# Optimization experiments

Hardware: AMD Instinct MI355X
Metric: run time of the kernel (lower is better)

## Reference

```python
import jax, jax.numpy as jnp
import numpy as np

# Per-layer (in_dim, hidden) for the 6 stacked LSTM layers:
# rnn_inp: (1,64),(64,64),(64,64); rnn_out: (64,1),(1,1),(1,1)
_LAYER_DIMS = [(1, 64), (64, 64), (64, 64), (64, 1), (1, 1), (1, 1)]
_LAYER_NAMES = ['a0', 'a1', 'a2', 'b0', 'b1', 'b2']


def _lstm_layer(x, w_ih, w_hh, b_ih, b_hh):
    """Single unidirectional LSTM layer, PyTorch gate order (i, f, g, o).
    x: [B, T, Din]; w_ih: [4H, Din]; w_hh: [4H, H]; biases: [4H]. Returns [B, T, H]."""
    H = w_hh.shape[1]
    B = x.shape[0]
    # Input projection for all timesteps at once (one big GEMM).
    pre = jnp.einsum('btd,gd->btg', x, w_ih) + b_ih + b_hh  # [B, T, 4H]
    pre_t = jnp.swapaxes(pre, 0, 1)  # [T, B, 4H]

    def step(carry, xt):
        h, c = carry
        gates = xt + h @ w_hh.T  # [B, 4H]
        i, f, g, o = jnp.split(gates, 4, axis=-1)
        i = jax.nn.sigmoid(i)
        f = jax.nn.sigmoid(f)
        g = jnp.tanh(g)
        o = jax.nn.sigmoid(o)
        c = f * c + i * g
        h = o * jnp.tanh(c)
        return (h, c), h

    h0 = jnp.zeros((B, H), x.dtype)
    (_, _), hs = jax.lax.scan(step, (h0, h0), pre_t)  # hs: [T, B, H]
    return jnp.swapaxes(hs, 0, 1)


def setup_inputs() -> dict:
    key = jax.random.key(0)
    B, T = 256, 512
    inp = {}
    k, key = jax.random.split(key)
    inp['x'] = jax.random.normal(k, (B, T, 1), dtype=jnp.float32)
    for name, (din, h) in zip(_LAYER_NAMES, _LAYER_DIMS):
        s = 1.0 / np.sqrt(h)  # PyTorch LSTM init scale U(-1/sqrt(H), 1/sqrt(H))
        k1, k2, k3, k4, key = jax.random.split(key, 5)
        inp[f'w_ih_{name}'] = jax.random.uniform(k1, (4 * h, din), jnp.float32, -s, s)
        inp[f'w_hh_{name}'] = jax.random.uniform(k2, (4 * h, h), jnp.float32, -s, s)
        inp[f'b_ih_{name}'] = jax.random.uniform(k3, (4 * h,), jnp.float32, -s, s)
        inp[f'b_hh_{name}'] = jax.random.uniform(k4, (4 * h,), jnp.float32, -s, s)
    return inp


def reference(x,
              w_ih_a0, w_hh_a0, b_ih_a0, b_hh_a0,
              w_ih_a1, w_hh_a1, b_ih_a1, b_hh_a1,
              w_ih_a2, w_hh_a2, b_ih_a2, b_hh_a2,
              w_ih_b0, w_hh_b0, b_ih_b0, b_hh_b0,
              w_ih_b1, w_hh_b1, b_ih_b1, b_hh_b1,
              w_ih_b2, w_hh_b2, b_ih_b2, b_hh_b2):
    layers = [
        (w_ih_a0, w_hh_a0, b_ih_a0, b_hh_a0),
        (w_ih_a1, w_hh_a1, b_ih_a1, b_hh_a1),
        (w_ih_a2, w_hh_a2, b_ih_a2, b_hh_a2),
        (w_ih_b0, w_hh_b0, b_ih_b0, b_hh_b0),
        (w_ih_b1, w_hh_b1, b_ih_b1, b_hh_b1),
        (w_ih_b2, w_hh_b2, b_ih_b2, b_hh_b2),
    ]
    h = x
    for w_ih, w_hh, b_ih, b_hh in layers:
        h = _lstm_layer(h, w_ih, w_hh, b_ih, b_hh)
    # activation between the two LSTM stacks is identity (activation_type='identity')
    return h  # [B, T, 1]
```

## Files before the change

### kernel.cpp

```cpp
#include <hip/hip_runtime.h>


#define BB 256
#define TT 512
#define CH 8
#define NS 16

typedef _Float16 v2h __attribute__((ext_vector_type(2)));

__device__ __forceinline__ float sig_(float x) {
  return __builtin_amdgcn_rcpf(1.f + __builtin_amdgcn_exp2f(-1.44269504f * x));
}
__device__ __forceinline__ float tanh_(float x) {
  return __builtin_fmaf(2.f, __builtin_amdgcn_rcpf(1.f + __builtin_amdgcn_exp2f(-2.88539008f * x)), -1.f);
}

template <int K>
__device__ __forceinline__ float qb_(float v) {
  return __int_as_float(__builtin_amdgcn_update_dpp(
      0, __float_as_int(v), (K | (K << 2) | (K << 4) | (K << 6)), 0xF, 0xF, true));
}

__device__ __forceinline__ void ldsbar_() {
  asm volatile("s_waitcnt lgkmcnt(0)\n\ts_barrier" ::: "memory");
}

#if __has_builtin(__builtin_amdgcn_fdot2)
#define FDOT2(acc, a, b) (acc) = __builtin_amdgcn_fdot2((a), (b), (acc), false)
#else
#define FDOT2(acc, a, b) \
  (acc) = __builtin_fmaf((float)(a)[0], (float)(b)[0], \
          __builtin_fmaf((float)(a)[1], (float)(b)[1], (acc)))
#endif
#define KEEPP(a) asm volatile("" : "+v"(a))
#define PIN16(w)                                                            \
  do {                                                                      \
    _Pragma("unroll") for (int _i = 0; _i < 16; ++_i) KEEPP((w)[_i]);       \
  } while (0)

__device__ __forceinline__ v2h bc2h_(int v) { return __builtin_bit_cast(v2h, v); }
__device__ __forceinline__ int pk2_(float x, float y) {
  return __builtin_bit_cast(int, v2h{(_Float16)x, (_Float16)y});
}

__device__ __forceinline__ void load_h64(const _Float16* p, v2h hv[32]) {
  const int4* hp = reinterpret_cast<const int4*>(p);
#pragma unroll
  for (int i = 0; i < 8; ++i) {
    int4 blk = hp[i];
    hv[4 * i + 0] = bc2h_(blk.x);
    hv[4 * i + 1] = bc2h_(blk.y);
    hv[4 * i + 2] = bc2h_(blk.z);
    hv[4 * i + 3] = bc2h_(blk.w);
  }
}

__device__ __forceinline__ void load_row_pair(const float* src, v2h lo[16], v2h hi[16]) {
  const float4* p = reinterpret_cast<const float4*>(src);
#pragma unroll
  for (int i = 0; i < 8; ++i) {
    float4 v = p[i];
    lo[2 * i]     = v2h{(_Float16)v.x, (_Float16)v.y};
    lo[2 * i + 1] = v2h{(_Float16)v.z, (_Float16)v.w};
  }
#pragma unroll
  for (int i = 0; i < 8; ++i) {
    float4 v = p[8 + i];
    hi[2 * i]     = v2h{(_Float16)v.x, (_Float16)v.y};
    hi[2 * i + 1] = v2h{(_Float16)v.z, (_Float16)v.w};
  }
}

__device__ __forceinline__ void load_rec_w(const float* W, int lane,
                                           v2h wt[4][16], unsigned char* wl) {
#pragma unroll
  for (int q = 0; q < 4; ++q) {
    const int row = q * 64 + lane;
    const float4* p = reinterpret_cast<const float4*>(W + row * 64);
#pragma unroll
    for (int i = 0; i < 8; ++i) {
      float4 v = p[i];
      wt[q][2 * i]     = v2h{(_Float16)v.x, (_Float16)v.y};
      wt[q][2 * i + 1] = v2h{(_Float16)v.z, (_Float16)v.w};
    }
#pragma unroll
    for (int i = 0; i < 4; ++i) {
      float4 va = p[8 + 2 * i], vb = p[9 + 2 * i];
      int4 blk;
      blk.x = pk2_(va.x, va.y); blk.y = pk2_(va.z, va.w);
      blk.z = pk2_(vb.x, vb.y); blk.w = pk2_(vb.z, vb.w);
      *reinterpret_cast<int4*>(wl + row * 80 + i * 16) = blk;
    }
  }
}

__device__ __forceinline__ void dot4full_(const v2h wt[4][16],
                                          const unsigned char* wl, int lane,
                                          const v2h hv[32],
                                          float& p0, float& p1, float& p2, float& p3) {
  float a0 = p0, a1 = p1, a2 = p2, a3 = p3;
  float b0 = 0.f, b1 = 0.f, b2 = 0.f, b3 = 0.f;
#pragma unroll
  for (int j = 0; j < 16; j += 2) {
    FDOT2(a0, wt[0][j], hv[j]);         FDOT2(a1, wt[1][j], hv[j]);
    FDOT2(a2, wt[2][j], hv[j]);         FDOT2(a3, wt[3][j], hv[j]);
    FDOT2(b0, wt[0][j + 1], hv[j + 1]); FDOT2(b1, wt[1][j + 1], hv[j + 1]);
    FDOT2(b2, wt[2][j + 1], hv[j + 1]); FDOT2(b3, wt[3][j + 1], hv[j + 1]);
  }
  const int rb0 = lane * 80, rb1 = (64 + lane) * 80,
            rb2 = (128 + lane) * 80, rb3 = (192 + lane) * 80;
#pragma unroll
  for (int jb = 0; jb < 4; ++jb) {
    int4 w0 = *reinterpret_cast<const int4*>(wl + rb0 + jb * 16);
    int4 w1 = *reinterpret_cast<const int4*>(wl + rb1 + jb * 16);
    int4 w2 = *reinterpret_cast<const int4*>(wl + rb2 + jb * 16);
    int4 w3 = *reinterpret_cast<const int4*>(wl + rb3 + jb * 16);
    const int h0 = 16 + jb * 4;
    FDOT2(a0, bc2h_(w0.x), hv[h0 + 0]); FDOT2(b0, bc2h_(w0.y), hv[h0 + 1]);
    FDOT2(a0, bc2h_(w0.z), hv[h0 + 2]); FDOT2(b0, bc2h_(w0.w), hv[h0 + 3]);
    FDOT2(a1, bc2h_(w1.x), hv[h0 + 0]); FDOT2(b1, bc2h_(w1.y), hv[h0 + 1]);
    FDOT2(a1, bc2h_(w1.z), hv[h0 + 2]); FDOT2(b1, bc2h_(w1.w), hv[h0 + 3]);
    FDOT2(a2, bc2h_(w2.x), hv[h0 + 0]); FDOT2(b2, bc2h_(w2.y), hv[h0 + 1]);
    FDOT2(a2, bc2h_(w2.z), hv[h0 + 2]); FDOT2(b2, bc2h_(w2.w), hv[h0 + 3]);
    FDOT2(a3, bc2h_(w3.x), hv[h0 + 0]); FDOT2(b3, bc2h_(w3.y), hv[h0 + 1]);
    FDOT2(a3, bc2h_(w3.z), hv[h0 + 2]); FDOT2(b3, bc2h_(w3.w), hv[h0 + 3]);
  }
  p0 = a0 + b0; p1 = a1 + b1; p2 = a2 + b2; p3 = a3 + b3;
}

__device__ __forceinline__ void dot2g_(const v2h* wa_lo, const v2h* wa_hi,
                                       const v2h* wb_lo, const v2h* wb_hi,
                                       const v2h hv[32], float& p0, float& p1) {
  float a0 = 0.f, a1 = 0.f, b0 = 0.f, b1 = 0.f;
#pragma unroll
  for (int j = 0; j < 16; j += 2) {
    FDOT2(a0, wa_lo[j], hv[j]);          FDOT2(b0, wa_lo[j + 1], hv[j + 1]);
    FDOT2(a0, wa_hi[j], hv[16 + j]);     FDOT2(b0, wa_hi[j + 1], hv[17 + j]);
    FDOT2(a1, wb_lo[j], hv[j]);          FDOT2(b1, wb_lo[j + 1], hv[j + 1]);
    FDOT2(a1, wb_hi[j], hv[16 + j]);     FDOT2(b1, wb_hi[j + 1], hv[17 + j]);
  }
  p0 = a0 + b0; p1 = a1 + b1;
}

__global__ __attribute__((amdgpu_flat_work_group_size(512, 512),
                          amdgpu_waves_per_eu(2, 2)))
void lstm_pipe_k(
    const float* __restrict__ x,
    const float* __restrict__ wih_a0, const float* __restrict__ whh_a0,
    const float* __restrict__ bih_a0, const float* __restrict__ bhh_a0,
    const float* __restrict__ wih_a1, const float* __restrict__ whh_a1,
    const float* __restrict__ bih_a1, const float* __restrict__ bhh_a1,
    const float* __restrict__ wih_a2, const float* __restrict__ whh_a2,
    const float* __restrict__ bih_a2, const float* __restrict__ bhh_a2,
    const float* __restrict__ wih_b0, const float* __restrict__ whh_b0,
    const float* __restrict__ bih_b0, const float* __restrict__ bhh_b0,
    const float* __restrict__ wih_b1, const float* __restrict__ whh_b1,
    const float* __restrict__ bih_b1, const float* __restrict__ bhh_b1,
    const float* __restrict__ wih_b2, const float* __restrict__ whh_b2,
    const float* __restrict__ bih_b2, const float* __restrict__ bhh_b2,
    float* __restrict__ out)
{
  const int b = blockIdx.x;
  const int tid = threadIdx.x;
  const int wave = tid >> 6;
  const int lane = tid & 63;

  __shared__ __align__(16) _Float16 hh[3][NS][64];
  __shared__ __align__(16) float pj[2][NS][256];
  __shared__ __align__(16) unsigned char wlds[3][256 * 80];
  __shared__ float xs[TT];

  for (int i = tid; i < TT; i += 512) xs[i] = x[(size_t)b * TT + i];
  for (int i = tid; i < 3 * NS * 64 / 2; i += 512) reinterpret_cast<int*>(hh)[i] = 0;

  v2h wt[4][16];
  float bias[4] = {0.f, 0.f, 0.f, 0.f};
  float wi0_[4] = {0.f, 0.f, 0.f, 0.f};
  float whb0[4] = {}, wi1b[4] = {}, wh1b[4] = {}, bb1[4] = {},
        wi2b[4] = {}, wh2b[4] = {}, bb2[4] = {};

  if (wave == 0) {
    load_rec_w(whh_a0, lane, wt, &wlds[0][0]);
#pragma unroll
    for (int q = 0; q < 4; ++q) {
      const int row = q * 64 + lane;
      bias[q] = bih_a0[row] + bhh_a0[row];
      wi0_[q] = wih_a0[row];
    }
    PIN16(wt[0]); PIN16(wt[1]); PIN16(wt[2]); PIN16(wt[3]);
  } else if (wave == 1) {
    load_rec_w(whh_a1, lane, wt, &wlds[1][0]);
#pragma unroll
    for (int q = 0; q < 4; ++q) {
      const int row = q * 64 + lane;
      bias[q] = bih_a1[row] + bhh_a1[row];
    }
    PIN16(wt[0]); PIN16(wt[1]); PIN16(wt[2]); PIN16(wt[3]);
  } else if (wave == 2) {
    load_rec_w(whh_a2, lane, wt, &wlds[2][0]);
#pragma unroll
    for (int q = 0; q < 4; ++q) {
      const int row = q * 64 + lane;
      bias[q] = bih_a2[row] + bhh_a2[row];
    }
    PIN16(wt[0]); PIN16(wt[1]); PIN16(wt[2]); PIN16(wt[3]);
  } else if (wave == 3) {
    const int q = lane & 3;
    load_row_pair(wih_b0 + q * 64, wt[0], wt[1]);
    bias[0] = bih_b0[q] + bhh_b0[q];
#pragma unroll
    for (int k = 0; k < 4; ++k) {
      whb0[k] = whh_b0[k];
      wi1b[k] = wih_b1[k]; wh1b[k] = whh_b1[k]; bb1[k] = bih_b1[k] + bhh_b1[k];
      wi2b[k] = wih_b2[k]; wh2b[k] = whh_b2[k]; bb2[k] = bih_b2[k] + bhh_b2[k];
    }
    PIN16(wt[0]); PIN16(wt[1]);
  } else if (wave == 4) {
    load_row_pair(wih_a1 + (0 * 64 + lane) * 64, wt[0], wt[1]);
    load_row_pair(wih_a1 + (1 * 64 + lane) * 64, wt[2], wt[3]);
    PIN16(wt[0]); PIN16(wt[1]); PIN16(wt[2]); PIN16(wt[3]);
  } else if (wave == 5) {
    load_row_pair(wih_a1 + (2 * 64 + lane) * 64, wt[0], wt[1]);
    load_row_pair(wih_a1 + (3 * 64 + lane) * 64, wt[2], wt[3]);
    PIN16(wt[0]); PIN16(wt[1]); PIN16(wt[2]); PIN16(wt[3]);
  } else if (wave == 6) {
    load_row_pair(wih_a2 + (0 * 64 + lane) * 64, wt[0], wt[1]);
    load_row_pair(wih_a2 + (1 * 64 + lane) * 64, wt[2], wt[3]);
    PIN16(wt[0]); PIN16(wt[1]); PIN16(wt[2]); PIN16(wt[3]);
  } else {
    load_row_pair(wih_a2 + (2 * 64 + lane) * 64, wt[0], wt[1]);
    load_row_pair(wih_a2 + (3 * 64 + lane) * 64, wt[2], wt[3]);
    PIN16(wt[0]); PIN16(wt[1]); PIN16(wt[2]); PIN16(wt[3]);
  }
  __syncthreads();

  float c = 0.f;
  float h0b = 0.f, c0b = 0.f, h1b = 0.f, c1b = 0.f, h2b = 0.f, c2b = 0.f;

  const int NE = TT / CH + 5;
  for (int e = 0; e < NE; ++e) {
    if (wave == 0) {
      const int t0 = e * CH;
      if (t0 < TT) {
        __builtin_amdgcn_s_setprio(1);
        for (int s = 0; s < CH; ++s) {
          const int t = t0 + s;
          v2h hv[32];
          load_h64(&hh[0][(t + NS - 1) & (NS - 1)][0], hv);
          const float xv = xs[t];
          float p0 = bias[0], p1 = bias[1], p2 = bias[2], p3 = bias[3];
          dot4full_(wt, &wlds[0][0], lane, hv, p0, p1, p2, p3);
          p0 = __builtin_fmaf(wi0_[0], xv, p0);
          p1 = __builtin_fmaf(wi0_[1], xv, p1);
          p2 = __builtin_fmaf(wi0_[2], xv, p2);
          p3 = __builtin_fmaf(wi0_[3], xv, p3);
          float gi = sig_(p0), gf = sig_(p1), gg = tanh_(p2), go = sig_(p3);
          c = __builtin_fmaf(gf, c, gi * gg);
          hh[0][t & (NS - 1)][lane] = (_Float16)(go * tanh_(c));
        }
        __builtin_amdgcn_s_setprio(0);
      }
    } else if (wave == 1) {
      const int t0 = (e - 2) * CH;
      if (t0 >= 0 && t0 < TT) {
        __builtin_amdgcn_s_setprio(1);
        for (int s = 0; s < CH; ++s) {
          const int t = t0 + s;
          v2h hv[32];
          load_h64(&hh[1][(t + NS - 1) & (NS - 1)][0], hv);
          float4 pr = *reinterpret_cast<const float4*>(&pj[0][t & (NS - 1)][lane * 4]);
          float p0 = bias[0], p1 = bias[1], p2 = bias[2], p3 = bias[3];
          dot4full_(wt, &wlds[1][0], lane, hv, p0, p1, p2, p3);
          p0 += pr.x; p1 += pr.y; p2 += pr.z; p3 += pr.w;
          float gi = sig_(p0), gf = sig_(p1), gg = tanh_(p2), go = sig_(p3);
          c = __builtin_fmaf(gf, c, gi * gg);
          hh[1][t & (NS - 1)][lane] = (_Float16)(go * tanh_(c));
        }
        __builtin_amdgcn_s_setprio(0);
      }
    } else if (wave == 2) {
      const int t0 = (e - 4) * CH;
      if (t0 >= 0 && t0 < TT) {
        __builtin_amdgcn_s_setprio(1);
        for (int s = 0; s < CH; ++s) {
          const int t = t0 + s;
          v2h hv[32];
          load_h64(&hh[2][(t + NS - 1) & (NS - 1)][0], hv);
          float4 pr = *reinterpret_cast<const float4*>(&pj[1][t & (NS - 1)][lane * 4]);
          float p0 = bias[0], p1 = bias[1], p2 = bias[2], p3 = bias[3];
          dot4full_(wt, &wlds[2][0], lane, hv, p0, p1, p2, p3);
          p0 += pr.x; p1 += pr.y; p2 += pr.z; p3 += pr.w;
          float gi = sig_(p0), gf = sig_(p1), gg = tanh_(p2), go = sig_(p3);
          c = __builtin_fmaf(gf, c, gi * gg);
          hh[2][t & (NS - 1)][lane] = (_Float16)(go * tanh_(c));
        }
        __builtin_amdgcn_s_setprio(0);
      }
    } else if (wave == 3) {
      const int t0 = (e - 5) * CH;
      if (t0 >= 0 && t0 < TT) {
        for (int s = 0; s < CH; ++s) {
          const int t = t0 + s;
          v2h hv[32];
          load_h64(&hh[2][t & (NS - 1)][0], hv);
          float pga = bias[0], pgb = 0.f;
#pragma unroll
          for (int j = 0; j < 16; ++j) {
            FDOT2(pga, wt[0][j], hv[j]);
            FDOT2(pgb, wt[1][j], hv[16 + j]);
          }
          float pg = pga + pgb;
          float p_i = qb_<0>(pg), p_f = qb_<1>(pg), p_g = qb_<2>(pg), p_o = qb_<3>(pg);
          float i0 = sig_(__builtin_fmaf(whb0[0], h0b, p_i));
          float f0 = sig_(__builtin_fmaf(whb0[1], h0b, p_f));
          float g0 = tanh_(__builtin_fmaf(whb0[2], h0b, p_g));
          float o0 = sig_(__builtin_fmaf(whb0[3], h0b, p_o));
          c0b = __builtin_fmaf(f0, c0b, i0 * g0);
          h0b = o0 * tanh_(c0b);
          float i1 = sig_(bb1[0] + __builtin_fmaf(wi1b[0], h0b, wh1b[0] * h1b));
          float f1 = sig_(bb1[1] + __builtin_fmaf(wi1b[1], h0b, wh1b[1] * h1b));
          float g1 = tanh_(bb1[2] + __builtin_fmaf(wi1b[2], h0b, wh1b[2] * h1b));
          float o1 = sig_(bb1[3] + __builtin_fmaf(wi1b[3], h0b, wh1b[3] * h1b));
          c1b = __builtin_fmaf(f1, c1b, i1 * g1);
          h1b = o1 * tanh_(c1b);
          float i2 = sig_(bb2[0] + __builtin_fmaf(wi2b[0], h1b, wh2b[0] * h2b));
          float f2 = sig_(bb2[1] + __builtin_fmaf(wi2b[1], h1b, wh2b[1] * h2b));
          float g2 = tanh_(bb2[2] + __builtin_fmaf(wi2b[2], h1b, wh2b[2] * h2b));
          float o2 = sig_(bb2[3] + __builtin_fmaf(wi2b[3], h1b, wh2b[3] * h2b));
          c2b = __builtin_fmaf(f2, c2b, i2 * g2);
          h2b = o2 * tanh_(c2b);
          if (lane == 0) out[(size_t)b * TT + t] = h2b;
        }
      }
    } else if (wave == 4) {
      const int t0 = (e - 1) * CH;
      if (t0 >= 0 && t0 < TT) {
        for (int s = 0; s < CH; ++s) {
          const int t = t0 + s;
          v2h hv[32];
          load_h64(&hh[0][t & (NS - 1)][0], hv);
          float p0, p1;
          dot2g_(wt[0], wt[1], wt[2], wt[3], hv, p0, p1);
          *reinterpret_cast<float2*>(&pj[0][t & (NS - 1)][lane * 4]) = float2{p0, p1};
        }
      }
    } else if (wave == 5) {
      const int t0 = (e - 1) * CH;
      if (t0 >= 0 && t0 < TT) {
        for (int s = 0; s < CH; ++s) {
          const int t = t0 + s;
          v2h hv[32];
          load_h64(&hh[0][t & (NS - 1)][0], hv);
          float p2, p3;
          dot2g_(wt[0], wt[1], wt[2], wt[3], hv, p2, p3);
          *reinterpret_cast<float2*>(&pj[0][t & (NS - 1)][lane * 4 + 2]) = float2{p2, p3};
        }
      }
    } else if (wave == 6) {
      const int t0 = (e - 3) * CH;
      if (t0 >= 0 && t0 < TT) {
        for (int s = 0; s < CH; ++s) {
          const int t = t0 + s;
          v2h hv[32];
          load_h64(&hh[1][t & (NS - 1)][0], hv);
          float p0, p1;
          dot2g_(wt[0], wt[1], wt[2], wt[3], hv, p0, p1);
          *reinterpret_cast<float2*>(&pj[1][t & (NS - 1)][lane * 4]) = float2{p0, p1};
        }
      }
    } else {
      const int t0 = (e - 3) * CH;
      if (t0 >= 0 && t0 < TT) {
        for (int s = 0; s < CH; ++s) {
          const int t = t0 + s;
          v2h hv[32];
          load_h64(&hh[1][t & (NS - 1)][0], hv);
          float p2, p3;
          dot2g_(wt[0], wt[1], wt[2], wt[3], hv, p2, p3);
          *reinterpret_cast<float2*>(&pj[1][t & (NS - 1)][lane * 4 + 2]) = float2{p2, p3};
        }
      }
    }
    ldsbar_();
  }
}

extern "C" void kernel_launch(void* const* d_in, const int* in_sizes, int n_in,
                              void* d_out, int out_size, void* d_ws, size_t ws_size,
                              hipStream_t stream) {
  const float* x      = (const float*)d_in[0];
  const float* wih_a0 = (const float*)d_in[1];
  const float* whh_a0 = (const float*)d_in[2];
  const float* bih_a0 = (const float*)d_in[3];
  const float* bhh_a0 = (const float*)d_in[4];
  const float* wih_a1 = (const float*)d_in[5];
  const float* whh_a1 = (const float*)d_in[6];
  const float* bih_a1 = (const float*)d_in[7];
  const float* bhh_a1 = (const float*)d_in[8];
  const float* wih_a2 = (const float*)d_in[9];
  const float* whh_a2 = (const float*)d_in[10];
  const float* bih_a2 = (const float*)d_in[11];
  const float* bhh_a2 = (const float*)d_in[12];
  const float* wih_b0 = (const float*)d_in[13];
  const float* whh_b0 = (const float*)d_in[14];
  const float* bih_b0 = (const float*)d_in[15];
  const float* bhh_b0 = (const float*)d_in[16];
  const float* wih_b1 = (const float*)d_in[17];
  const float* whh_b1 = (const float*)d_in[18];
  const float* bih_b1 = (const float*)d_in[19];
  const float* bhh_b1 = (const float*)d_in[20];
  const float* wih_b2 = (const float*)d_in[21];
  const float* whh_b2 = (const float*)d_in[22];
  const float* bih_b2 = (const float*)d_in[23];
  const float* bhh_b2 = (const float*)d_in[24];
  float* out = (float*)d_out;

  lstm_pipe_k<<<BB, 512, 0, stream>>>(
      x,
      wih_a0, whh_a0, bih_a0, bhh_a0,
      wih_a1, whh_a1, bih_a1, bhh_a1,
      wih_a2, whh_a2, bih_a2, bhh_a2,
      wih_b0, whh_b0, bih_b0, bhh_b0,
      wih_b1, whh_b1, bih_b1, bhh_b1,
      wih_b2, whh_b2, bih_b2, bhh_b2,
      out);
}
```

Baseline: 410.4 us.

## Compute recurrent LSTM matvec with MFMA 16x16x32 f16 instead of fdot2

The three 64-hidden recurrent waves now hold the whole W_hh in registers as MFMA B fragments (16 tiles x 2 k-chunks). Each step does 32 MFMA instructions against the broadcast previous h, then selects each lane's four gate values from the accumulators. The shared-memory weight spill and the fdot2 chains go away. In exchange, 15 of 16 rows of each MFMA are wasted work, MFMA latency sits on the serial recurrence path, and register pressure grows.

```diff
diff --git a/kernel.cpp b/kernel.cpp
--- a/kernel.cpp
+++ b/kernel.cpp
@@ -7,6 +7,8 @@
 #define NS 16
 
 typedef _Float16 v2h __attribute__((ext_vector_type(2)));
+typedef _Float16 v8h __attribute__((ext_vector_type(8)));
+typedef float v4f __attribute__((ext_vector_type(4)));
 
 __device__ __forceinline__ float sig_(float x) {
   return __builtin_amdgcn_rcpf(1.f + __builtin_amdgcn_exp2f(-1.44269504f * x));
@@ -39,9 +41,6 @@
   } while (0)
 
 __device__ __forceinline__ v2h bc2h_(int v) { return __builtin_bit_cast(v2h, v); }
-__device__ __forceinline__ int pk2_(float x, float y) {
-  return __builtin_bit_cast(int, v2h{(_Float16)x, (_Float16)y});
-}
 
 __device__ __forceinline__ void load_h64(const _Float16* p, v2h hv[32]) {
   const int4* hp = reinterpret_cast<const int4*>(p);
@@ -71,61 +70,41 @@
   }
 }
 
-__device__ __forceinline__ void load_rec_w(const float* W, int lane,
-                                           v2h wt[4][16], unsigned char* wl) {
-#pragma unroll
-  for (int q = 0; q < 4; ++q) {
-    const int row = q * 64 + lane;
-    const float4* p = reinterpret_cast<const float4*>(W + row * 64);
-#pragma unroll
-    for (int i = 0; i < 8; ++i) {
-      float4 v = p[i];
-      wt[q][2 * i]     = v2h{(_Float16)v.x, (_Float16)v.y};
-      wt[q][2 * i + 1] = v2h{(_Float16)v.z, (_Float16)v.w};
-    }
-#pragma unroll
-    for (int i = 0; i < 4; ++i) {
-      float4 va = p[8 + 2 * i], vb = p[9 + 2 * i];
-      int4 blk;
-      blk.x = pk2_(va.x, va.y); blk.y = pk2_(va.z, va.w);
-      blk.z = pk2_(vb.x, vb.y); blk.w = pk2_(vb.z, vb.w);
-      *reinterpret_cast<int4*>(wl + row * 80 + i * 16) = blk;
-    }
-  }
-}
-
-__device__ __forceinline__ void dot4full_(const v2h wt[4][16],
-                                          const unsigned char* wl, int lane,
-                                          const v2h hv[32],
-                                          float& p0, float& p1, float& p2, float& p3) {
-  float a0 = p0, a1 = p1, a2 = p2, a3 = p3;
-  float b0 = 0.f, b1 = 0.f, b2 = 0.f, b3 = 0.f;
-#pragma unroll
-  for (int j = 0; j < 16; j += 2) {
-    FDOT2(a0, wt[0][j], hv[j]);         FDOT2(a1, wt[1][j], hv[j]);
-    FDOT2(a2, wt[2][j], hv[j]);         FDOT2(a3, wt[3][j], hv[j]);
-    FDOT2(b0, wt[0][j + 1], hv[j + 1]); FDOT2(b1, wt[1][j + 1], hv[j + 1]);
-    FDOT2(b2, wt[2][j + 1], hv[j + 1]); FDOT2(b3, wt[3][j + 1], hv[j + 1]);
-  }
-  const int rb0 = lane * 80, rb1 = (64 + lane) * 80,
-            rb2 = (128 + lane) * 80, rb3 = (192 + lane) * 80;
-#pragma unroll
-  for (int jb = 0; jb < 4; ++jb) {
-    int4 w0 = *reinterpret_cast<const int4*>(wl + rb0 + jb * 16);
-    int4 w1 = *reinterpret_cast<const int4*>(wl + rb1 + jb * 16);
-    int4 w2 = *reinterpret_cast<const int4*>(wl + rb2 + jb * 16);
-    int4 w3 = *reinterpret_cast<const int4*>(wl + rb3 + jb * 16);
-    const int h0 = 16 + jb * 4;
-    FDOT2(a0, bc2h_(w0.x), hv[h0 + 0]); FDOT2(b0, bc2h_(w0.y), hv[h0 + 1]);
-    FDOT2(a0, bc2h_(w0.z), hv[h0 + 2]); FDOT2(b0, bc2h_(w0.w), hv[h0 + 3]);
-    FDOT2(a1, bc2h_(w1.x), hv[h0 + 0]); FDOT2(b1, bc2h_(w1.y), hv[h0 + 1]);
-    FDOT2(a1, bc2h_(w1.z), hv[h0 + 2]); FDOT2(b1, bc2h_(w1.w), hv[h0 + 3]);
-    FDOT2(a2, bc2h_(w2.x), hv[h0 + 0]); FDOT2(b2, bc2h_(w2.y), hv[h0 + 1]);
-    FDOT2(a2, bc2h_(w2.z), hv[h0 + 2]); FDOT2(b2, bc2h_(w2.w), hv[h0 + 3]);
-    FDOT2(a3, bc2h_(w3.x), hv[h0 + 0]); FDOT2(b3, bc2h_(w3.y), hv[h0 + 1]);
-    FDOT2(a3, bc2h_(w3.z), hv[h0 + 2]); FDOT2(b3, bc2h_(w3.w), hv[h0 + 3]);
-  }
-  p0 = a0 + b0; p1 = a1 + b1; p2 = a2 + b2; p3 = a3 + b3;
+__device__ __forceinline__ v8h ldbfrag_(const float* W, int t, int kc, int lane) {
+  const int row = 16 * t + (lane & 15);
+  const float* p = W + row * 64 + 32 * kc + 4 * (lane >> 4);
+  float4 fa = *reinterpret_cast<const float4*>(p);
+  float4 fb = *reinterpret_cast<const float4*>(p + 16);
+  return v8h{(_Float16)fa.x, (_Float16)fa.y, (_Float16)fa.z, (_Float16)fa.w,
+             (_Float16)fb.x, (_Float16)fb.y, (_Float16)fb.z, (_Float16)fb.w};
+}
+
+__device__ __forceinline__ void mfma_matvec_(const v8h bfr[16][2],
+                                             const _Float16* hprev, int lane,
+                                             float p[4]) {
+  const char* hp = reinterpret_cast<const char*>(hprev);
+  const int off = 8 * (lane >> 4);
+  int2 r00 = *reinterpret_cast<const int2*>(hp + off);
+  int2 r01 = *reinterpret_cast<const int2*>(hp + off + 32);
+  int2 r10 = *reinterpret_cast<const int2*>(hp + off + 64);
+  int2 r11 = *reinterpret_cast<const int2*>(hp + off + 96);
+  v8h A0 = __builtin_bit_cast(v8h, int4{r00.x, r00.y, r01.x, r01.y});
+  v8h A1 = __builtin_bit_cast(v8h, int4{r10.x, r10.y, r11.x, r11.y});
+  const v4f z = {0.f, 0.f, 0.f, 0.f};
+  v4f acc[16];
+#pragma unroll
+  for (int t = 0; t < 16; ++t) {
+    v4f d = __builtin_amdgcn_mfma_f32_16x16x32_f16(A0, bfr[t][0], z, 0, 0, 0);
+    acc[t] = __builtin_amdgcn_mfma_f32_16x16x32_f16(A1, bfr[t][1], d, 0, 0, 0);
+  }
+  const int q = lane >> 4;
+  const bool s0 = q & 1, s1 = q & 2;
+#pragma unroll
+  for (int g = 0; g < 4; ++g) {
+    float v01 = s0 ? acc[4 * g + 1][0] : acc[4 * g + 0][0];
+    float v23 = s0 ? acc[4 * g + 3][0] : acc[4 * g + 2][0];
+    p[g] = s1 ? v23 : v01;
+  }
 }
 
 __device__ __forceinline__ void dot2g_(const v2h* wa_lo, const v2h* wa_hi,
@@ -167,12 +146,12 @@
 
   __shared__ __align__(16) _Float16 hh[3][NS][64];
   __shared__ __align__(16) float pj[2][NS][256];
-  __shared__ __align__(16) unsigned char wlds[3][256 * 80];
   __shared__ float xs[TT];
 
   for (int i = tid; i < TT; i += 512) xs[i] = x[(size_t)b * TT + i];
   for (int i = tid; i < 3 * NS * 64 / 2; i += 512) reinterpret_cast<int*>(hh)[i] = 0;
 
+  v8h bfr[16][2];
   v2h wt[4][16];
   float bias[4] = {0.f, 0.f, 0.f, 0.f};
   float wi0_[4] = {0.f, 0.f, 0.f, 0.f};
@@ -180,30 +159,33 @@
         wi2b[4] = {}, wh2b[4] = {}, bb2[4] = {};
 
   if (wave == 0) {
-    load_rec_w(whh_a0, lane, wt, &wlds[0][0]);
+#pragma unroll
+    for (int t = 0; t < 16; ++t) {
+      bfr[t][0] = ldbfrag_(whh_a0, t, 0, lane);
+      bfr[t][1] = ldbfrag_(whh_a0, t, 1, lane);
+    }
 #pragma unroll
     for (int q = 0; q < 4; ++q) {
       const int row = q * 64 + lane;
       bias[q] = bih_a0[row] + bhh_a0[row];
       wi0_[q] = wih_a0[row];
     }
-    PIN16(wt[0]); PIN16(wt[1]); PIN16(wt[2]); PIN16(wt[3]);
   } else if (wave == 1) {
-    load_rec_w(whh_a1, lane, wt, &wlds[1][0]);
-#pragma unroll
-    for (int q = 0; q < 4; ++q) {
-      const int row = q * 64 + lane;
-      bias[q] = bih_a1[row] + bhh_a1[row];
-    }
-    PIN16(wt[0]); PIN16(wt[1]); PIN16(wt[2]); PIN16(wt[3]);
+#pragma unroll
+    for (int t = 0; t < 16; ++t) {
+      bfr[t][0] = ldbfrag_(whh_a1, t, 0, lane);
+      bfr[t][1] = ldbfrag_(whh_a1, t, 1, lane);
+    }
+#pragma unroll
+    for (int q = 0; q < 4; ++q) bias[q] = bih_a1[q * 64 + lane] + bhh_a1[q * 64 + lane];
   } else if (wave == 2) {
-    load_rec_w(whh_a2, lane, wt, &wlds[2][0]);
-#pragma unroll
-    for (int q = 0; q < 4; ++q) {
-      const int row = q * 64 + lane;
-      bias[q] = bih_a2[row] + bhh_a2[row];
-    }
-    PIN16(wt[0]); PIN16(wt[1]); PIN16(wt[2]); PIN16(wt[3]);
+#pragma unroll
+    for (int t = 0; t < 16; ++t) {
+      bfr[t][0] = ldbfrag_(whh_a2, t, 0, lane);
+      bfr[t][1] = ldbfrag_(whh_a2, t, 1, lane);
+    }
+#pragma unroll
+    for (int q = 0; q < 4; ++q) bias[q] = bih_a2[q * 64 + lane] + bhh_a2[q * 64 + lane];
   } else if (wave == 3) {
     const int q = lane & 3;
     load_row_pair(wih_b0 + q * 64, wt[0], wt[1]);
@@ -245,15 +227,13 @@
         __builtin_amdgcn_s_setprio(1);
         for (int s = 0; s < CH; ++s) {
           const int t = t0 + s;
-          v2h hv[32];
-          load_h64(&hh[0][(t + NS - 1) & (NS - 1)][0], hv);
           const float xv = xs[t];
-          float p0 = bias[0], p1 = bias[1], p2 = bias[2], p3 = bias[3];
-          dot4full_(wt, &wlds[0][0], lane, hv, p0, p1, p2, p3);
-          p0 = __builtin_fmaf(wi0_[0], xv, p0);
-          p1 = __builtin_fmaf(wi0_[1], xv, p1);
-          p2 = __builtin_fmaf(wi0_[2], xv, p2);
-          p3 = __builtin_fmaf(wi0_[3], xv, p3);
+          float p[4];
+          mfma_matvec_(bfr, &hh[0][(t + NS - 1) & (NS - 1)][0], lane, p);
+          float p0 = __builtin_fmaf(wi0_[0], xv, p[0] + bias[0]);
+          float p1 = __builtin_fmaf(wi0_[1], xv, p[1] + bias[1]);
+          float p2 = __builtin_fmaf(wi0_[2], xv, p[2] + bias[2]);
+          float p3 = __builtin_fmaf(wi0_[3], xv, p[3] + bias[3]);
           float gi = sig_(p0), gf = sig_(p1), gg = tanh_(p2), go = sig_(p3);
           c = __builtin_fmaf(gf, c, gi * gg);
           hh[0][t & (NS - 1)][lane] = (_Float16)(go * tanh_(c));
@@ -266,12 +246,13 @@
         __builtin_amdgcn_s_setprio(1);
         for (int s = 0; s < CH; ++s) {
           const int t = t0 + s;
-          v2h hv[32];
-          load_h64(&hh[1][(t + NS - 1) & (NS - 1)][0], hv);
           float4 pr = *reinterpret_cast<const float4*>(&pj[0][t & (NS - 1)][lane * 4]);
-          float p0 = bias[0], p1 = bias[1], p2 = bias[2], p3 = bias[3];
-          dot4full_(wt, &wlds[1][0], lane, hv, p0, p1, p2, p3);
-          p0 += pr.x; p1 += pr.y; p2 += pr.z; p3 += pr.w;
+          float p[4];
+          mfma_matvec_(bfr, &hh[1][(t + NS - 1) & (NS - 1)][0], lane, p);
+          float p0 = p[0] + bias[0] + pr.x;
+          float p1 = p[1] + bias[1] + pr.y;
+          float p2 = p[2] + bias[2] + pr.z;
+          float p3 = p[3] + bias[3] + pr.w;
           float gi = sig_(p0), gf = sig_(p1), gg = tanh_(p2), go = sig_(p3);
           c = __builtin_fmaf(gf, c, gi * gg);
           hh[1][t & (NS - 1)][lane] = (_Float16)(go * tanh_(c));
@@ -284,12 +265,13 @@
         __builtin_amdgcn_s_setprio(1);
         for (int s = 0; s < CH; ++s) {
           const int t = t0 + s;
-          v2h hv[32];
-          load_h64(&hh[2][(t + NS - 1) & (NS - 1)][0], hv);
           float4 pr = *reinterpret_cast<const float4*>(&pj[1][t & (NS - 1)][lane * 4]);
-          float p0 = bias[0], p1 = bias[1], p2 = bias[2], p3 = bias[3];
-          dot4full_(wt, &wlds[2][0], lane, hv, p0, p1, p2, p3);
-          p0 += pr.x; p1 += pr.y; p2 += pr.z; p3 += pr.w;
+          float p[4];
+          mfma_matvec_(bfr, &hh[2][(t + NS - 1) & (NS - 1)][0], lane, p);
+          float p0 = p[0] + bias[0] + pr.x;
+          float p1 = p[1] + bias[1] + pr.y;
+          float p2 = p[2] + bias[2] + pr.z;
+          float p3 = p[3] + bias[3] + pr.w;
           float gi = sig_(p0), gf = sig_(p1), gg = tanh_(p2), go = sig_(p3);
           c = __builtin_fmaf(gf, c, gi * gg);
           hh[2][t & (NS - 1)][lane] = (_Float16)(go * tanh_(c));
```

After: 583.8 us. +42.2%, slower.

## Replace block-wide barrier pipeline with per-wave LDS progress flags

Applied to the files above, without the earlier changes.

The lockstep epoch loop, which ended every chunk with s_barrier across all eight waves, is replaced by per-wave progress counters in shared memory. Each wave spins on acquire loads until its producers have finished the chunk it needs and its consumers have freed ring slots, then posts its own progress with a release store. This lets each pipeline stage run ahead independently instead of waiting for the slowest wave every chunk, which should shorten the critical path through the wave-0 recurrence. The cost is busy-wait polling that takes issue slots on the SIMDs, plus the risk of ordering bugs in the ring-buffer dependencies.

```diff
diff --git a/kernel.cpp b/kernel.cpp
--- a/kernel.cpp
+++ b/kernel.cpp
@@ -5,6 +5,7 @@
 #define TT 512
 #define CH 8
 #define NS 16
+#define NW (TT / CH)
 
 typedef _Float16 v2h __attribute__((ext_vector_type(2)));
 
@@ -19,10 +20,6 @@
 __device__ __forceinline__ float qb_(float v) {
   return __int_as_float(__builtin_amdgcn_update_dpp(
       0, __float_as_int(v), (K | (K << 2) | (K << 4) | (K << 6)), 0xF, 0xF, true));
-}
-
-__device__ __forceinline__ void ldsbar_() {
-  asm volatile("s_waitcnt lgkmcnt(0)\n\ts_barrier" ::: "memory");
 }
 
 #if __has_builtin(__builtin_amdgcn_fdot2)
@@ -36,6 +33,17 @@
 #define PIN16(w)                                                            \
   do {                                                                      \
     _Pragma("unroll") for (int _i = 0; _i < 16; ++_i) KEEPP((w)[_i]);       \
+  } while (0)
+
+#define WAITP(i, v)                                                           \
+  while (__hip_atomic_load(&prog[i], __ATOMIC_ACQUIRE,                        \
+                           __HIP_MEMORY_SCOPE_WORKGROUP) < (v)) {}
+#define POSTP(i, v)                                                           \
+  do {                                                                        \
+    asm volatile("s_waitcnt lgkmcnt(0)" ::: "memory");                        \
+    if (lane == 0)                                                            \
+      __hip_atomic_store(&prog[i], (v), __ATOMIC_RELEASE,                     \
+                         __HIP_MEMORY_SCOPE_WORKGROUP);                       \
   } while (0)
 
 __device__ __forceinline__ v2h bc2h_(int v) { return __builtin_bit_cast(v2h, v); }
@@ -169,9 +177,11 @@
   __shared__ __align__(16) float pj[2][NS][256];
   __shared__ __align__(16) unsigned char wlds[3][256 * 80];
   __shared__ float xs[TT];
+  __shared__ int prog[8];
 
   for (int i = tid; i < TT; i += 512) xs[i] = x[(size_t)b * TT + i];
   for (int i = tid; i < 3 * NS * 64 / 2; i += 512) reinterpret_cast<int*>(hh)[i] = 0;
+  if (tid < 8) prog[tid] = 0;
 
   v2h wt[4][16];
   float bias[4] = {0.f, 0.f, 0.f, 0.f};
@@ -191,18 +201,12 @@
   } else if (wave == 1) {
     load_rec_w(whh_a1, lane, wt, &wlds[1][0]);
 #pragma unroll
-    for (int q = 0; q < 4; ++q) {
-      const int row = q * 64 + lane;
-      bias[q] = bih_a1[row] + bhh_a1[row];
-    }
+    for (int q = 0; q < 4; ++q) bias[q] = bih_a1[q * 64 + lane] + bhh_a1[q * 64 + lane];
     PIN16(wt[0]); PIN16(wt[1]); PIN16(wt[2]); PIN16(wt[3]);
   } else if (wave == 2) {
     load_rec_w(whh_a2, lane, wt, &wlds[2][0]);
 #pragma unroll
-    for (int q = 0; q < 4; ++q) {
-      const int row = q * 64 + lane;
-      bias[q] = bih_a2[row] + bhh_a2[row];
-    }
+    for (int q = 0; q < 4; ++q) bias[q] = bih_a2[q * 64 + lane] + bhh_a2[q * 64 + lane];
     PIN16(wt[0]); PIN16(wt[1]); PIN16(wt[2]); PIN16(wt[3]);
   } else if (wave == 3) {
     const int q = lane & 3;
@@ -237,151 +241,169 @@
   float c = 0.f;
   float h0b = 0.f, c0b = 0.f, h1b = 0.f, c1b = 0.f, h2b = 0.f, c2b = 0.f;
 
-  const int NE = TT / CH + 5;
-  for (int e = 0; e < NE; ++e) {
-    if (wave == 0) {
-      const int t0 = e * CH;
-      if (t0 < TT) {
-        __builtin_amdgcn_s_setprio(1);
-        for (int s = 0; s < CH; ++s) {
-          const int t = t0 + s;
-          v2h hv[32];
-          load_h64(&hh[0][(t + NS - 1) & (NS - 1)][0], hv);
-          const float xv = xs[t];
-          float p0 = bias[0], p1 = bias[1], p2 = bias[2], p3 = bias[3];
-          dot4full_(wt, &wlds[0][0], lane, hv, p0, p1, p2, p3);
-          p0 = __builtin_fmaf(wi0_[0], xv, p0);
-          p1 = __builtin_fmaf(wi0_[1], xv, p1);
-          p2 = __builtin_fmaf(wi0_[2], xv, p2);
-          p3 = __builtin_fmaf(wi0_[3], xv, p3);
-          float gi = sig_(p0), gf = sig_(p1), gg = tanh_(p2), go = sig_(p3);
-          c = __builtin_fmaf(gf, c, gi * gg);
-          hh[0][t & (NS - 1)][lane] = (_Float16)(go * tanh_(c));
+  if (wave == 0) {
+    __builtin_amdgcn_s_setprio(1);
+    for (int k = 0; k < NW; ++k) {
+      if (k >= 2) { WAITP(4, k - 1); WAITP(5, k - 1); }
+      const int t0 = k * CH;
+      for (int s = 0; s < CH; ++s) {
+        const int t = t0 + s;
+        v2h hv[32];
+        load_h64(&hh[0][(t + NS - 1) & (NS - 1)][0], hv);
+        const float xv = xs[t];
+        float p0 = bias[0], p1 = bias[1], p2 = bias[2], p3 = bias[3];
+        dot4full_(wt, &wlds[0][0], lane, hv, p0, p1, p2, p3);
+        p0 = __builtin_fmaf(wi0_[0], xv, p0);
+        p1 = __builtin_fmaf(wi0_[1], xv, p1);
+        p2 = __builtin_fmaf(wi0_[2], xv, p2);
+        p3 = __builtin_fmaf(wi0_[3], xv, p3);
+        float gi = sig_(p0), gf = sig_(p1), gg = tanh_(p2), go = sig_(p3);
+        c = __builtin_fmaf(gf, c, gi * gg);
+        hh[0][t & (NS - 1)][lane] = (_Float16)(go * tanh_(c));
+      }
+      POSTP(0, k + 1);
+    }
+    __builtin_amdgcn_s_setprio(0);
+  } else if (wave == 1) {
+    __builtin_amdgcn_s_setprio(1);
+    for (int k = 0; k < NW; ++k) {
+      WAITP(4, k + 1); WAITP(5, k + 1);
+      if (k >= 2) { WAITP(6, k - 1); WAITP(7, k - 1); }
+      const int t0 = k * CH;
+      for (int s = 0; s < CH; ++s) {
+        const int t = t0 + s;
+        v2h hv[32];
+        load_h64(&hh[1][(t + NS - 1) & (NS - 1)][0], hv);
+        float4 pr = *reinterpret_cast<const float4*>(&pj[0][t & (NS - 1)][lane * 4]);
+        float p0 = bias[0], p1 = bias[1], p2 = bias[2], p3 = bias[3];
+        dot4full_(wt, &wlds[1][0], lane, hv, p0, p1, p2, p3);
+        p0 += pr.x; p1 += pr.y; p2 += pr.z; p3 += pr.w;
+        float gi = sig_(p0), gf = sig_(p1), gg = tanh_(p2), go = sig_(p3);
+        c = __builtin_fmaf(gf, c, gi * gg);
+        hh[1][t & (NS - 1)][lane] = (_Float16)(go * tanh_(c));
+      }
+      POSTP(1, k + 1);
+    }
+    __builtin_amdgcn_s_setprio(0);
+  } else if (wave == 2) {
+    __builtin_amdgcn_s_setprio(1);
+    for (int k = 0; k < NW; ++k) {
+      WAITP(6, k + 1); WAITP(7, k + 1);
+      if (k >= 2) { WAITP(3, k - 1); }
+      const int t0 = k * CH;
+      for (int s = 0; s < CH; ++s) {
+        const int t = t0 + s;
+        v2h hv[32];
+        load_h64(&hh[2][(t + NS - 1) & (NS - 1)][0], hv);
+        float4 pr = *reinterpret_cast<const float4*>(&pj[1][t & (NS - 1)][lane * 4]);
+        float p0 = bias[0], p1 = bias[1], p2 = bias[2], p3 = bias[3];
+        dot4full_(wt, &wlds[2][0], lane, hv, p0, p1, p2, p3);
+        p0 += pr.x; p1 += pr.y; p2 += pr.z; p3 += pr.w;
+        float gi = sig_(p0), gf = sig_(p1), gg = tanh_(p2), go = sig_(p3);
+        c = __builtin_fmaf(gf, c, gi * gg);
+        hh[2][t & (NS - 1)][lane] = (_Float16)(go * tanh_(c));
+      }
+      POSTP(2, k + 1);
+    }
+    __builtin_amdgcn_s_setprio(0);
+  } else if (wave == 3) {
+    for (int k = 0; k < NW; ++k) {
+      WAITP(2, k + 1);
+      const int t0 = k * CH;
+      for (int s = 0; s < CH; ++s) {
+        const int t = t0 + s;
+        v2h hv[32];
+        load_h64(&hh[2][t & (NS - 1)][0], hv);
+        float pga = bias[0], pgb = 0.f;
+#pragma unroll
+        for (int j = 0; j < 16; ++j) {
+          FDOT2(pga, wt[0][j], hv[j]);
+          FDOT2(pgb, wt[1][j], hv[16 + j]);
         }
-        __builtin_amdgcn_s_setprio(0);
-      }
-    } else if (wave == 1) {
-      const int t0 = (e - 2) * CH;
-      if (t0 >= 0 && t0 < TT) {
-        __builtin_amdgcn_s_setprio(1);
-        for (int s = 0; s < CH; ++s) {
-          const int t = t0 + s;
-          v2h hv[32];
-          load_h64(&hh[1][(t + NS - 1) & (NS - 1)][0], hv);
-          float4 pr = *reinterpret_cast<const float4*>(&pj[0][t & (NS - 1)][lane * 4]);
-          float p0 = bias[0], p1 = bias[1], p2 = bias[2], p3 = bias[3];
-          dot4full_(wt, &wlds[1][0], lane, hv, p0, p1, p2, p3);
-          p0 += pr.x; p1 += pr.y; p2 += pr.z; p3 += pr.w;
-          float gi = sig_(p0), gf = sig_(p1), gg = tanh_(p2), go = sig_(p3);
-          c = __builtin_fmaf(gf, c, gi * gg);
-          hh[1][t & (NS - 1)][lane] = (_Float16)(go * tanh_(c));
-        }
-        __builtin_amdgcn_s_setprio(0);
-      }
-    } else if (wave == 2) {
-      const int t0 = (e - 4) * CH;
-      if (t0 >= 0 && t0 < TT) {
-        __builtin_amdgcn_s_setprio(1);
-        for (int s = 0; s < CH; ++s) {
-          const int t = t0 + s;
-          v2h hv[32];
-          load_h64(&hh[2][(t + NS - 1) & (NS - 1)][0], hv);
-          float4 pr = *reinterpret_cast<const float4*>(&pj[1][t & (NS - 1)][lane * 4]);
-          float p0 = bias[0], p1 = bias[1], p2 = bias[2], p3 = bias[3];
-          dot4full_(wt, &wlds[2][0], lane, hv, p0, p1, p2, p3);
-          p0 += pr.x; p1 += pr.y; p2 += pr.z; p3 += pr.w;
-          float gi = sig_(p0), gf = sig_(p1), gg = tanh_(p2), go = sig_(p3);
-          c = __builtin_fmaf(gf, c, gi * gg);
-          hh[2][t & (NS - 1)][lane] = (_Float16)(go * tanh_(c));
-        }
-        __builtin_amdgcn_s_setprio(0);
-      }
-    } else if (wave == 3) {
-      const int t0 = (e - 5) * CH;
-      if (t0 >= 0 && t0 < TT) {
-        for (int s = 0; s < CH; ++s) {
-          const int t = t0 + s;
-          v2h hv[32];
-          load_h64(&hh[2][t & (NS - 1)][0], hv);
-          float pga = bias[0], pgb = 0.f;
-#pragma unroll
-          for (int j = 0; j < 16; ++j) {
-            FDOT2(pga, wt[0][j], hv[j]);
-            FDOT2(pgb, wt[1][j], hv[16 + j]);
-          }
-          float pg = pga + pgb;
-          float p_i = qb_<0>(pg), p_f = qb_<1>(pg), p_g = qb_<2>(pg), p_o = qb_<3>(pg);
-          float i0 = sig_(__builtin_fmaf(whb0[0], h0b, p_i));
-          float f0 = sig_(__builtin_fmaf(whb0[1], h0b, p_f));
-          float g0 = tanh_(__builtin_fmaf(whb0[2], h0b, p_g));
-          float o0 = sig_(__builtin_fmaf(whb0[3], h0b, p_o));
-          c0b = __builtin_fmaf(f0, c0b, i0 * g0);
-          h0b = o0 * tanh_(c0b);
-          float i1 = sig_(bb1[0] + __builtin_fmaf(wi1b[0], h0b, wh1b[0] * h1b));
-          float f1 = sig_(bb1[1] + __builtin_fmaf(wi1b[1], h0b, wh1b[1] * h1b));
-          float g1 = tanh_(bb1[2] + __builtin_fmaf(wi1b[2], h0b, wh1b[2] * h1b));
-          float o1 = sig_(bb1[3] + __builtin_fmaf(wi1b[3], h0b, wh1b[3] * h1b));
-          c1b = __builtin_fmaf(f1, c1b, i1 * g1);
-          h1b = o1 * tanh_(c1b);
-          float i2 = sig_(bb2[0] + __builtin_fmaf(wi2b[0], h1b, wh2b[0] * h2b));
-          float f2 = sig_(bb2[1] + __builtin_fmaf(wi2b[1], h1b, wh2b[1] * h2b));
-          float g2 = tanh_(bb2[2] + __builtin_fmaf(wi2b[2], h1b, wh2b[2] * h2b));
-          float o2 = sig_(bb2[3] + __builtin_fmaf(wi2b[3], h1b, wh2b[3] * h2b));
-          c2b = __builtin_fmaf(f2, c2b, i2 * g2);
-          h2b = o2 * tanh_(c2b);
-          if (lane == 0) out[(size_t)b * TT + t] = h2b;
-        }
-      }
-    } else if (wave == 4) {
-      const int t0 = (e - 1) * CH;
-      if (t0 >= 0 && t0 < TT) {
-        for (int s = 0; s < CH; ++s) {
-          const int t = t0 + s;
-          v2h hv[32];
-          load_h64(&hh[0][t & (NS - 1)][0], hv);
-          float p0, p1;
-          dot2g_(wt[0], wt[1], wt[2], wt[3], hv, p0, p1);
-          *reinterpret_cast<float2*>(&pj[0][t & (NS - 1)][lane * 4]) = float2{p0, p1};
-        }
-      }
-    } else if (wave == 5) {
-      const int t0 = (e - 1) * CH;
-      if (t0 >= 0 && t0 < TT) {
-        for (int s = 0; s < CH; ++s) {
-          const int t = t0 + s;
-          v2h hv[32];
-          load_h64(&hh[0][t & (NS - 1)][0], hv);
-          float p2, p3;
-          dot2g_(wt[0], wt[1], wt[2], wt[3], hv, p2, p3);
-          *reinterpret_cast<float2*>(&pj[0][t & (NS - 1)][lane * 4 + 2]) = float2{p2, p3};
-        }
-      }
-    } else if (wave == 6) {
-      const int t0 = (e - 3) * CH;
-      if (t0 >= 0 && t0 < TT) {
-        for (int s = 0; s < CH; ++s) {
-          const int t = t0 + s;
-          v2h hv[32];
-          load_h64(&hh[1][t & (NS - 1)][0], hv);
-          float p0, p1;
-          dot2g_(wt[0], wt[1], wt[2], wt[3], hv, p0, p1);
-          *reinterpret_cast<float2*>(&pj[1][t & (NS - 1)][lane * 4]) = float2{p0, p1};
-        }
-      }
-    } else {
-      const int t0 = (e - 3) * CH;
-      if (t0 >= 0 && t0 < TT) {
-        for (int s = 0; s < CH; ++s) {
-          const int t = t0 + s;
-          v2h hv[32];
-          load_h64(&hh[1][t & (NS - 1)][0], hv);
-          float p2, p3;
-          dot2g_(wt[0], wt[1], wt[2], wt[3], hv, p2, p3);
-          *reinterpret_cast<float2*>(&pj[1][t & (NS - 1)][lane * 4 + 2]) = float2{p2, p3};
-        }
-      }
-    }
-    ldsbar_();
+        float pg = pga + pgb;
+        float p_i = qb_<0>(pg), p_f = qb_<1>(pg), p_g = qb_<2>(pg), p_o = qb_<3>(pg);
+        float i0 = sig_(__builtin_fmaf(whb0[0], h0b, p_i));
+        float f0 = sig_(__builtin_fmaf(whb0[1], h0b, p_f));
+        float g0 = tanh_(__builtin_fmaf(whb0[2], h0b, p_g));
+        float o0 = sig_(__builtin_fmaf(whb0[3], h0b, p_o));
+        c0b = __builtin_fmaf(f0, c0b, i0 * g0);
+        h0b = o0 * tanh_(c0b);
+        float i1 = sig_(bb1[0] + __builtin_fmaf(wi1b[0], h0b, wh1b[0] * h1b));
+        float f1 = sig_(bb1[1] + __builtin_fmaf(wi1b[1], h0b, wh1b[1] * h1b));
+        float g1 = tanh_(bb1[2] + __builtin_fmaf(wi1b[2], h0b, wh1b[2] * h1b));
+        float o1 = sig_(bb1[3] + __builtin_fmaf(wi1b[3], h0b, wh1b[3] * h1b));
+        c1b = __builtin_fmaf(f1, c1b, i1 * g1);
+        h1b = o1 * tanh_(c1b);
+        float i2 = sig_(bb2[0] + __builtin_fmaf(wi2b[0], h1b, wh2b[0] * h2b));
+        float f2 = sig_(bb2[1] + __builtin_fmaf(wi2b[1], h1b, wh2b[1] * h2b));
+        float g2 = tanh_(bb2[2] + __builtin_fmaf(wi2b[2], h1b, wh2b[2] * h2b));
+        float o2 = sig_(bb2[3] + __builtin_fmaf(wi2b[3], h1b, wh2b[3] * h2b));
+        c2b = __builtin_fmaf(f2, c2b, i2 * g2);
+        h2b = o2 * tanh_(c2b);
+        if (lane == 0) out[(size_t)b * TT + t] = h2b;
+      }
+      POSTP(3, k + 1);
+    }
+  } else if (wave == 4) {
+    for (int k = 0; k < NW; ++k) {
+      WAITP(0, k + 1);
+      if (k >= 2) { WAITP(1, k - 1); }
+      const int t0 = k * CH;
+      for (int s = 0; s < CH; ++s) {
+        const int t = t0 + s;
+        v2h hv[32];
+        load_h64(&hh[0][t & (NS - 1)][0], hv);
+        float p0, p1;
+        dot2g_(wt[0], wt[1], wt[2], wt[3], hv, p0, p1);
+        *reinterpret_cast<float2*>(&pj[0][t & (NS - 1)][lane * 4]) = float2{p0, p1};
+      }
+      POSTP(4, k + 1);
+    }
+  } else if (wave == 5) {
+    for (int k = 0; k < NW; ++k) {
+      WAITP(0, k + 1);
+      if (k >= 2) { WAITP(1, k - 1); }
+      const int t0 = k * CH;
+      for (int s = 0; s < CH; ++s) {
+        const int t = t0 + s;
+        v2h hv[32];
+        load_h64(&hh[0][t & (NS - 1)][0], hv);
+        float p2, p3;
+        dot2g_(wt[0], wt[1], wt[2], wt[3], hv, p2, p3);
+        *reinterpret_cast<float2*>(&pj[0][t & (NS - 1)][lane * 4 + 2]) = float2{p2, p3};
+      }
+      POSTP(5, k + 1);
+    }
+  } else if (wave == 6) {
+    for (int k = 0; k < NW; ++k) {
+      WAITP(1, k + 1);
+      if (k >= 2) { WAITP(2, k - 1); }
+      const int t0 = k * CH;
+      for (int s = 0; s < CH; ++s) {
+        const int t = t0 + s;
+        v2h hv[32];
+        load_h64(&hh[1][t & (NS - 1)][0], hv);
+        float p0, p1;
+        dot2g_(wt[0], wt[1], wt[2], wt[3], hv, p0, p1);
+        *reinterpret_cast<float2*>(&pj[1][t & (NS - 1)][lane * 4]) = float2{p0, p1};
+      }
+      POSTP(6, k + 1);
+    }
+  } else {
+    for (int k = 0; k < NW; ++k) {
+      WAITP(1, k + 1);
+      if (k >= 2) { WAITP(2, k - 1); }
+      const int t0 = k * CH;
+      for (int s = 0; s < CH; ++s) {
+        const int t = t0 + s;
+        v2h hv[32];
+        load_h64(&hh[1][t & (NS - 1)][0], hv);
+        float p2, p3;
+        dot2g_(wt[0], wt[1], wt[2], wt[3], hv, p2, p3);
+        *reinterpret_cast<float2*>(&pj[1][t & (NS - 1)][lane * 4 + 2]) = float2{p2, p3};
+      }
+      POSTP(7, k + 1);
+    }
   }
 }
 
```

After: 401.0 us. 1.02x faster.
